# Kernel tuning notes

Hardware: AMD Instinct MI355X
Metric: run time of the kernel (lower is better)

Reference implementation:

```python
import jax, jax.numpy as jnp
import numpy as np

N1, E1, D_IN, D_OUT = 100000, 1600000, 128, 128
N2, E2, NB = 1024, 200000, 30


def setup_inputs() -> dict:
    key = jax.random.key(0)
    ks = jax.random.split(key, 11)
    return {
        "x_g1": jax.random.normal(ks[0], (N1, D_IN), jnp.float32),
        "W_stc": jax.random.normal(ks[1], (D_IN, D_OUT), jnp.float32) / np.sqrt(D_IN),
        "b_stc": jax.random.normal(ks[2], (D_OUT,), jnp.float32) * 0.01,
        "x_g2": jax.random.normal(ks[3], (N2, N2), jnp.float32),
        "basis": jax.random.normal(ks[4], (NB, N2, N2), jnp.float32) / np.sqrt(N2 * NB),
        "att": jax.random.normal(ks[5], (E2, NB), jnp.float32),
        "root": jax.random.normal(ks[6], (N2, N2), jnp.float32) / np.sqrt(N2),
        "bias_rgcn": jax.random.normal(ks[7], (N2,), jnp.float32) * 0.01,
        "edge_index_g1": jax.random.randint(ks[8], (2, E1), 0, N1, jnp.int64),
        "edge_index_g2": jax.random.randint(ks[9], (2, E2), 0, N2, jnp.int64),
        "edge_type_g2": jax.random.randint(ks[10], (E2,), 0, E2, jnp.int64),
    }


def reference(x_g1, W_stc, b_stc, x_g2, basis, att, root, bias_rgcn,
              edge_index_g1, edge_index_g2, edge_type_g2):
    # ---- STCConv on G1: mean-aggregate neighbor features, then linear ----
    src1, dst1 = edge_index_g1[0], edge_index_g1[1]
    deg1 = jax.ops.segment_sum(jnp.ones((E1,), x_g1.dtype), dst1, num_segments=N1)
    agg1 = jax.ops.segment_sum(x_g1[src1], dst1, num_segments=N1)  # [N1, D_IN]
    agg1 = agg1 / jnp.maximum(deg1, 1.0)[:, None]
    h1 = jax.nn.relu(agg1 @ W_stc + b_stc)
    out1 = jax.nn.log_softmax(h1, axis=1)

    # ---- RGCNConv on G2 with basis decomposition: W_r = sum_b att[r,b] B_b ----
    src2, dst2 = edge_index_g2[0], edge_index_g2[1]
    deg2 = jnp.maximum(
        jax.ops.segment_sum(jnp.ones((E2,), x_g2.dtype), dst2, num_segments=N2), 1.0)
    x_src = x_g2[src2]            # [E2, N2] gathered source features
    coeff = att[edge_type_g2]     # [E2, NB] per-edge basis coefficients
    h2 = x_g2 @ root + bias_rgcn  # root/self transform
    # aggregate per basis first (cheap [N2,N2] matmul after scatter)
    for b in range(NB):
        S = jax.ops.segment_sum(x_src * coeff[:, b:b + 1], dst2, num_segments=N2)
        h2 = h2 + (S / deg2[:, None]) @ basis[b]
    h2 = jax.nn.relu(h2)
    out2 = jax.nn.log_softmax(h2, axis=1)
    return (out1, out2)
```

## Files before the change

### kernel.cpp

```cpp
#include <hip/hip_runtime.h>

typedef unsigned short u16;
typedef unsigned int u32;
typedef unsigned long long u64;
typedef __attribute__((ext_vector_type(8))) short short8;
typedef __attribute__((ext_vector_type(4))) float floatx4;

#define NBMAX 2048

__device__ __forceinline__ float b2f(u16 u) {
    u32 x = ((u32)u) << 16; float f; __builtin_memcpy(&f, &x, 4); return f;
}
__device__ __forceinline__ u16 f2b(float f) {
    u32 x; __builtin_memcpy(&x, &f, 4);
    u32 r = (x + 0x7fffu + ((x >> 16) & 1u)) >> 16;
    return (u16)r;
}
__device__ __forceinline__ float ldf(const void* p, long i, int isf) {
    return isf ? ((const float*)p)[i] : b2f(((const u16*)p)[i]);
}
__device__ __forceinline__ void stf(void* p, long i, float v, int isf) {
    if (isf) ((float*)p)[i] = v; else ((u16*)p)[i] = f2b(v);
}
__device__ __forceinline__ int ldidx(const int* w, long i, int is64) {
    return is64 ? w[2 * i] : w[i];
}
__device__ __forceinline__ void gload16(const u16* g, u16* l) {
    __builtin_amdgcn_global_load_lds((const __attribute__((address_space(1))) void*)g,
                                     (__attribute__((address_space(3))) void*)l, 16, 0, 0);
}

__global__ void detect_kernel(const u32* __restrict__ xw, const u32* __restrict__ iw,
                              int* __restrict__ flags) {
    int lane = threadIdx.x;
    u32 w = xw[lane];
    u32 b1 = (w >> 8) & 0x7f;
    int isbf = (b1 >= 0x38 && b1 <= 0x41) ? 1 : 0;
    int cbf = __popcll(__ballot(isbf));
    u32 hi = iw[2 * lane + 1];
    int cz = __popcll(__ballot(hi == 0u));
    if (lane == 0) {
        flags[0] = (cbf < 32) ? 1 : 0;
        flags[1] = (cz >= 56) ? 1 : 0;
    }
}


__global__ void count_kernel(const int* __restrict__ eiw, int E, int* __restrict__ cnt,
                             const int* __restrict__ flags) {
    int e = blockIdx.x * 256 + threadIdx.x;
    if (e < E) atomicAdd(&cnt[ldidx(eiw, (long)E + e, flags[1])], 1);
}

__global__ __launch_bounds__(256)
void bcount_kernel(const int* __restrict__ eiw, int E, int chunk,
                   int* __restrict__ bcnt, int NB, const int* __restrict__ flags) {
    __shared__ int h[NBMAX];
    int t = threadIdx.x;
    for (int i = t; i < NB; i += 256) h[i] = 0;
    __syncthreads();
    int is64 = flags[1];
    int lo = blockIdx.x * chunk;
    int hi = lo + chunk; if (hi > E) hi = E;
    for (int e = lo + t; e < hi; e += 256)
        atomicAdd(&h[ldidx(eiw, (long)E + e, is64) >> 7], 1);
    __syncthreads();
    for (int i = t; i < NB; i += 256)
        if (h[i]) atomicAdd(&bcnt[i], h[i]);
}

__global__ void bscan_kernel(const int* __restrict__ bcnt, int* __restrict__ boff,
                             int* __restrict__ bcur, int NB) {
    __shared__ int sm[1024];
    int t = threadIdx.x;
    int a = (2 * t < NB) ? bcnt[2 * t] : 0;
    int b = (2 * t + 1 < NB) ? bcnt[2 * t + 1] : 0;
    int s = a + b;
    sm[t] = s;
    __syncthreads();
    for (int o = 1; o < 1024; o <<= 1) {
        int x = (t >= o) ? sm[t - o] : 0;
        __syncthreads();
        sm[t] += x;
        __syncthreads();
    }
    int ex = sm[t] - s;
    if (2 * t < NB) { boff[2 * t] = ex; bcur[2 * t] = ex; }
    if (2 * t + 1 < NB) { boff[2 * t + 1] = ex + a; bcur[2 * t + 1] = ex + a; }
    if (t == 1023) boff[NB] = sm[1023];
}

__global__ __launch_bounds__(256)
void bscatter_kernel(const int* __restrict__ eiw, int E, int chunk,
                     int* __restrict__ bcur, int NB, u32* __restrict__ pair,
                     const int* __restrict__ flags) {
    __shared__ int h[NBMAX];
    __shared__ int cur[NBMAX];
    int t = threadIdx.x;
    for (int i = t; i < NB; i += 256) h[i] = 0;
    __syncthreads();
    int is64 = flags[1];
    int lo = blockIdx.x * chunk;
    int hi = lo + chunk; if (hi > E) hi = E;
    for (int e = lo + t; e < hi; e += 256)
        atomicAdd(&h[ldidx(eiw, (long)E + e, is64) >> 7], 1);
    __syncthreads();
    for (int i = t; i < NB; i += 256) {
        int c = h[i];
        h[i] = c ? atomicAdd(&bcur[i], c) : 0;
        cur[i] = 0;
    }
    __syncthreads();
    for (int e = lo + t; e < hi; e += 256) {
        int src = ldidx(eiw, e, is64);
        int d = ldidx(eiw, (long)E + e, is64);
        int b = d >> 7;
        int p = atomicAdd(&cur[b], 1);
        pair[h[b] + p] = ((u32)(d & 127) << 25) | (u32)src;
    }
}

__global__ __launch_bounds__(256)
void bucketfill2_kernel(const u32* __restrict__ pair, const int* __restrict__ boff,
                        int NB, int N1, int* __restrict__ off1, int* __restrict__ elist) {
    __shared__ int cnt[128], pre[128], soff[128], cur[128];
    int b = blockIdx.x, t = threadIdx.x;
    int lo = boff[b], hi = boff[b + 1];
    if (t < 128) cnt[t] = 0;
    __syncthreads();
    for (int i = lo + t; i < hi; i += 256)
        atomicAdd(&cnt[pair[i] >> 25], 1);
    __syncthreads();
    if (t < 128) pre[t] = cnt[t];
    __syncthreads();
    for (int o = 1; o < 128; o <<= 1) {
        int x = (t >= o && t < 128) ? pre[t - o] : 0;
        __syncthreads();
        if (t < 128) pre[t] += x;
        __syncthreads();
    }
    int d0 = b << 7;
    if (t < 128) {
        int s = lo + pre[t] - cnt[t];
        soff[t] = s;
        cur[t] = 0;
        if (d0 + t < N1) off1[d0 + t] = s;
    }
    if (b == NB - 1 && t == 0) off1[N1] = hi;
    __syncthreads();
    for (int i = lo + t; i < hi; i += 256) {
        u32 v = pair[i];
        int dl = v >> 25;
        int p = atomicAdd(&cur[dl], 1);
        elist[soff[dl] + p] = (int)(v & 0x1FFFFFFu);
    }
}

__global__ void scan_block_kernel(const int* __restrict__ in, int* __restrict__ out,
                                  int* __restrict__ bsum, int n) {
    __shared__ int sm[1024];
    int t = threadIdx.x;
    int i = blockIdx.x * 1024 + t;
    int v = (i < n) ? in[i] : 0;
    sm[t] = v;
    __syncthreads();
    for (int o = 1; o < 1024; o <<= 1) {
        int x = (t >= o) ? sm[t - o] : 0;
        __syncthreads();
        sm[t] += x;
        __syncthreads();
    }
    if (i < n) out[i] = sm[t] - v;
    if (t == 1023) bsum[blockIdx.x] = sm[1023];
}

__global__ void scan_small_kernel(int* __restrict__ bsum, int nb) {
    __shared__ int sm[128];
    int t = threadIdx.x;
    int v = (t < nb) ? bsum[t] : 0;
    sm[t] = v;
    __syncthreads();
    for (int o = 1; o < 128; o <<= 1) {
        int x = (t >= o) ? sm[t - o] : 0;
        __syncthreads();
        sm[t] += x;
        __syncthreads();
    }
    if (t < nb) bsum[t] = sm[t] - v;
}

__global__ void scan_add_kernel(int* __restrict__ off, const int* __restrict__ bsum,
                                int n, int total) {
    int i = blockIdx.x * 1024 + threadIdx.x;
    if (i < n) off[i] += bsum[blockIdx.x];
    if (i == 0) off[n] = total;
}

__global__ void fill_kernel(const int* __restrict__ eiw, int E, const int* __restrict__ off,
                            int* __restrict__ cur, int* __restrict__ elist,
                            const int* __restrict__ flags) {
    int e = blockIdx.x * 256 + threadIdx.x;
    if (e < E) {
        int is64 = flags[1];
        int d = ldidx(eiw, (long)E + e, is64);
        int p = atomicAdd(&cur[d], 1);
        elist[off[d] + p] = ldidx(eiw, e, is64);
    }
}

__global__ void fill2_kernel(const int* __restrict__ ei, const int* __restrict__ et, int E,
                             const int* __restrict__ off, int* __restrict__ cur,
                             u32* __restrict__ elist, const int* __restrict__ flags) {
    int e = blockIdx.x * 256 + threadIdx.x;
    if (e < E) {
        int is64 = flags[1];
        int s = ldidx(ei, e, is64);
        int d = ldidx(ei, (long)E + e, is64);
        int t = ldidx(et, e, is64);
        int p = atomicAdd(&cur[d], 1);
        elist[off[d] + p] = (u32)s | ((u32)t << 10);
    }
}

__global__ void cvt4_kernel(const void* __restrict__ in, u64* __restrict__ out, long n4,
                            const int* __restrict__ flags) {
    long i = (long)blockIdx.x * 256 + threadIdx.x;
    if (i >= n4) return;
    if (flags[0]) {
        float4 v = ((const float4*)in)[i];
        out[i] = (u64)f2b(v.x) | ((u64)f2b(v.y) << 16) | ((u64)f2b(v.z) << 32) |
                 ((u64)f2b(v.w) << 48);
    } else {
        out[i] = ((const u64*)in)[i];
    }
}

__global__ void agg_kernel(const void* __restrict__ xraw, const u32* __restrict__ xb,
                           const int* __restrict__ off, const int* __restrict__ elist,
                           u32* __restrict__ aggbf, int N, const int* __restrict__ flags,
                           int useXB) {
    int node = blockIdx.x * 4 + (threadIdx.x >> 6);
    if (node >= N) return;
    int lane = threadIdx.x & 63;
    int b = off[node], e = off[node + 1];
    float a0 = 0.f, a1 = 0.f, c0 = 0.f, c1 = 0.f;
    if (useXB) {
        int i = b;
        for (; i + 4 <= e; i += 4) {
            int s0 = elist[i], s1 = elist[i + 1], s2 = elist[i + 2], s3 = elist[i + 3];
            u32 v0 = xb[(long)s0 * 64 + lane];
            u32 v1 = xb[(long)s1 * 64 + lane];
            u32 v2 = xb[(long)s2 * 64 + lane];
            u32 v3 = xb[(long)s3 * 64 + lane];
            a0 += b2f((u16)(v0 & 0xffffu)) + b2f((u16)(v2 & 0xffffu));
            a1 += b2f((u16)(v0 >> 16)) + b2f((u16)(v2 >> 16));
            c0 += b2f((u16)(v1 & 0xffffu)) + b2f((u16)(v3 & 0xffffu));
            c1 += b2f((u16)(v1 >> 16)) + b2f((u16)(v3 >> 16));
        }
        for (; i < e; i++) {
            u32 v = xb[(long)elist[i] * 64 + lane];
            a0 += b2f((u16)(v & 0xffffu));
            a1 += b2f((u16)(v >> 16));
        }
        a0 += c0; a1 += c1;
    } else if (flags[0]) {
        const float* xf = (const float*)xraw;
        for (int i = b; i < e; i++) {
            long s = elist[i];
            a0 += xf[s * 128 + 2 * lane];
            a1 += xf[s * 128 + 2 * lane + 1];
        }
    } else {
        const u32* xu = (const u32*)xraw;
        for (int i = b; i < e; i++) {
            u32 v = xu[(long)elist[i] * 64 + lane];
            a0 += b2f((u16)(v & 0xffffu));
            a1 += b2f((u16)(v >> 16));
        }
    }
    int dg = e - b; if (dg < 1) dg = 1;
    float inv = 1.0f / (float)dg;
    aggbf[(long)node * 64 + lane] = (u32)f2b(a0 * inv) | ((u32)f2b(a1 * inv) << 16);
}

__global__ void transpose_kernel(const void* __restrict__ in, long inOff,
                                 u16* __restrict__ out, int R, int C,
                                 const int* __restrict__ flags) {
    __shared__ u16 tile[32][33];
    int isf = flags[0];
    int tx = threadIdx.x, ty = threadIdx.y;
    int x = blockIdx.x * 32 + tx;
#pragma unroll
    for (int i = 0; i < 4; i++) {
        int y = blockIdx.y * 32 + ty + i * 8;
        long idx = inOff + (long)y * C + x;
        tile[ty + i * 8][tx] = isf ? f2b(((const float*)in)[idx]) : ((const u16*)in)[idx];
    }
    __syncthreads();
    int x2 = blockIdx.y * 32 + tx;
#pragma unroll
    for (int i = 0; i < 4; i++) {
        int y2 = blockIdx.x * 32 + ty + i * 8;
        out[(long)y2 * R + x2] = tile[tx][ty + i * 8];
    }
}

__global__ __launch_bounds__(256)
void scatterA_lds_kernel(const u32* __restrict__ elist, const int* __restrict__ off,
                         const void* __restrict__ att, u16* __restrict__ Abf,
                         int b0, int CH, const int* __restrict__ flags) {
    __shared__ float sA[15 * 1024];
    const int d = blockIdx.x, t = threadIdx.x;
    const int b = off[d], e = off[d + 1];
    int cnt = e - b; if (cnt < 1) cnt = 1;
    const float inv = 1.0f / (float)cnt;
    const int tot = CH << 10;
    for (int i = t; i < tot; i += 256) sA[i] = 0.f;
    __syncthreads();
    const int isf = flags[0];
    for (int i = b + t; i < e; i += 256) {
        u32 v = elist[i];
        int s = v & 1023;
        long tb = (long)(v >> 10) * 30 + b0;
        for (int bb = 0; bb < CH; bb++)
            atomicAdd(&sA[(bb << 10) + s], ldf(att, tb + bb, isf) * inv);
    }
    __syncthreads();
    const long obase = (long)d * 256 + t;
    for (int bb = 0; bb < CH; bb++) {
        int base = (bb << 10) + (t << 2);
        u64 p = (u64)f2b(sA[base]) | ((u64)f2b(sA[base + 1]) << 16) |
                ((u64)f2b(sA[base + 2]) << 32) | ((u64)f2b(sA[base + 3]) << 48);
        ((u64*)Abf)[(long)bb * 262144 + obase] = p;
    }
}

template <int MODE>
__global__ __launch_bounds__(256)
void gemm_bt(const u16* __restrict__ A, long aBatch,
             const u16* __restrict__ BT,
             float* __restrict__ Cf, void* __restrict__ Cb,
             const void* __restrict__ bias, const int* __restrict__ flags,
             int M, int lda, int ldb, int ldc,
             int colOffDim, long cBatch, int kSplitStride, int kLen) {
    __shared__ u16 As[4096];
    __shared__ u16 Bs[4096];
    __shared__ float sred[2][2][128];
    const int t = threadIdx.x;
    const int gx = gridDim.x, gy = gridDim.y;
    const int nwg = gx * gy * gridDim.z;
    const int bid = blockIdx.x + gx * (blockIdx.y + gy * blockIdx.z);
    const int q = nwg >> 3, r = nwg & 7;
    const int xcd = bid & 7, idx = bid >> 3;
    const int nbid = (xcd < r ? xcd * (q + 1) : r * (q + 1) + (xcd - r) * q) + idx;
    const int bx = nbid % gx;
    const int by = (nbid / gx) % gy;
    const int bz = nbid / (gx * gy);

    const int isf = flags[0];
    A += (long)bz * aBatch;
    const int kBase = bz * kSplitStride;
    const int row0 = bx * 128;
    const int n0 = by * 128;
    const int lane = t & 63, wave = t >> 6;
    const int wrow = (wave >> 1) * 64, wcol = (wave & 1) * 64;
    const int quad = lane >> 4, l16 = lane & 15;

    long aoff[2], boff[2];
    u16 *ldsA[2], *ldsB[2];
#pragma unroll
    for (int h = 0; h < 2; h++) {
        int r2 = h * 64 + wave * 16 + (lane >> 2);
        int clog = (lane & 3) ^ ((r2 >> 1) & 3);
        int ga = row0 + r2; if (ga >= M) ga = M - 1;
        aoff[h] = (long)ga * lda + clog * 8;
        boff[h] = (long)(n0 + r2) * ldb + clog * 8;
        ldsA[h] = &As[(h * 64 + wave * 16) * 32];
        ldsB[h] = &Bs[(h * 64 + wave * 16) * 32];
    }
    int aidx[4], bidx[4];
#pragma unroll
    for (int i = 0; i < 4; i++) {
        int ra = wrow + i * 16 + l16;
        aidx[i] = ra * 32 + ((quad ^ ((ra >> 1) & 3)) * 8);
        int rb = wcol + i * 16 + l16;
        bidx[i] = rb * 32 + ((quad ^ ((rb >> 1) & 3)) * 8);
    }

    floatx4 acc[4][4];
#pragma unroll
    for (int i = 0; i < 4; i++)
#pragma unroll
        for (int j = 0; j < 4; j++)
            acc[i][j] = (floatx4){0.f, 0.f, 0.f, 0.f};

    for (int kt = kBase; kt < kBase + kLen; kt += 32) {
        __syncthreads();
#pragma unroll
        for (int h = 0; h < 2; h++) {
            gload16(A + aoff[h] + kt, ldsA[h]);
            gload16(BT + boff[h] + kt, ldsB[h]);
        }
        __syncthreads();
        short8 af[4], bfr[4];
#pragma unroll
        for (int i = 0; i < 4; i++) {
            af[i]  = *(const short8*)&As[aidx[i]];
            bfr[i] = *(const short8*)&Bs[bidx[i]];
        }
#pragma unroll
        for (int i = 0; i < 4; i++)
#pragma unroll
            for (int j = 0; j < 4; j++)
                acc[i][j] = __builtin_amdgcn_mfma_f32_16x16x32_bf16(af[i], bfr[j], acc[i][j], 0, 0, 0);
    }

    if (MODE == 0) {
        const int colhalf = wave & 1;
        float bv[4];
#pragma unroll
        for (int j = 0; j < 4; j++)
            bv[j] = ldf(bias, wcol + j * 16 + l16, isf);
        float Mp[4][4];
#pragma unroll
        for (int i = 0; i < 4; i++)
#pragma unroll
            for (int rr = 0; rr < 4; rr++) {
                float m = 0.f;
#pragma unroll
                for (int j = 0; j < 4; j++) {
                    float v = fmaxf(acc[i][j][rr] + bv[j], 0.f);
                    acc[i][j][rr] = v;
                    m = fmaxf(m, v);
                }
#pragma unroll
                for (int o = 1; o < 16; o <<= 1) m = fmaxf(m, __shfl_xor(m, o, 64));
                if (l16 == 0) sred[0][colhalf][wrow + i * 16 + quad * 4 + rr] = m;
            }
        __syncthreads();
#pragma unroll
        for (int i = 0; i < 4; i++)
#pragma unroll
            for (int rr = 0; rr < 4; rr++) {
                int r2 = wrow + i * 16 + quad * 4 + rr;
                Mp[i][rr] = fmaxf(sred[0][0][r2], sred[0][1][r2]);
                float s = 0.f;
#pragma unroll
                for (int j = 0; j < 4; j++) s += __expf(acc[i][j][rr] - Mp[i][rr]);
#pragma unroll
                for (int o = 1; o < 16; o <<= 1) s += __shfl_xor(s, o, 64);
                if (l16 == 0) sred[1][colhalf][r2] = s;
            }
        __syncthreads();
#pragma unroll
        for (int i = 0; i < 4; i++)
#pragma unroll
            for (int rr = 0; rr < 4; rr++) {
                int r2 = wrow + i * 16 + quad * 4 + rr;
                long crow = (long)row0 + r2;
                if (crow < M) {
                    float lg = __logf(sred[1][0][r2] + sred[1][1][r2]);
#pragma unroll
                    for (int j = 0; j < 4; j++)
                        stf(Cb, crow * 128 + wcol + j * 16 + l16,
                            acc[i][j][rr] - Mp[i][rr] - lg, isf);
                }
            }
        return;
    }

    const long colOff = (long)bz * colOffDim;
    float* Cfp = Cf ? Cf + (long)bz * cBatch : nullptr;
#pragma unroll
    for (int i = 0; i < 4; i++)
#pragma unroll
        for (int j = 0; j < 4; j++)
#pragma unroll
            for (int r2 = 0; r2 < 4; r2++) {
                long crow = row0 + wrow + i * 16 + quad * 4 + r2;
                long ccol = n0 + wcol + j * 16 + l16;
                float v = acc[i][j][r2];
                if (MODE == 1) {
                    ((u16*)Cb)[crow * ldc + colOff + ccol] = f2b(v);
                } else if (MODE == 2) {
                    Cfp[crow * ldc + ccol] = v + ldf(bias, ccol, isf);
                } else if (MODE == 3) {
                    Cfp[crow * ldc + ccol] += v;
                } else {
                    Cfp[crow * ldc + ccol] = v;
                }
            }
}

__global__ void softmax2_kernel(const float* __restrict__ Zr, const float* __restrict__ Zp,
                                void* __restrict__ out, long outOff, int nsplit,
                                const int* __restrict__ flags) {
    int row = blockIdx.x;
    int t = threadIdx.x;
    __shared__ float red[4];
    float4 v = ((const float4*)Zr)[(long)row * 256 + t];
    for (int s = 0; s < nsplit; s++) {
        float4 p = ((const float4*)Zp)[(long)s * 262144 + (long)row * 256 + t];
        v.x += p.x; v.y += p.y; v.z += p.z; v.w += p.w;
    }
    float z[4] = {fmaxf(v.x, 0.f), fmaxf(v.y, 0.f), fmaxf(v.z, 0.f), fmaxf(v.w, 0.f)};
    float m = fmaxf(fmaxf(z[0], z[1]), fmaxf(z[2], z[3]));
#pragma unroll
    for (int o = 1; o < 64; o <<= 1) m = fmaxf(m, __shfl_xor(m, o, 64));
    int wave = t >> 6, lane = t & 63;
    if (lane == 0) red[wave] = m;
    __syncthreads();
    m = fmaxf(fmaxf(red[0], red[1]), fmaxf(red[2], red[3]));
    __syncthreads();
    float s4 = __expf(z[0] - m) + __expf(z[1] - m) + __expf(z[2] - m) + __expf(z[3] - m);
#pragma unroll
    for (int o = 1; o < 64; o <<= 1) s4 += __shfl_xor(s4, o, 64);
    if (lane == 0) red[wave] = s4;
    __syncthreads();
    float lg = __logf(red[0] + red[1] + red[2] + red[3]);
    long base = outOff + (long)row * 1024 + t * 4;
    if (flags[0]) {
        float4 o = {z[0] - m - lg, z[1] - m - lg, z[2] - m - lg, z[3] - m - lg};
        ((float4*)out)[base >> 2] = o;
    } else {
        u64 p = (u64)f2b(z[0] - m - lg) | ((u64)f2b(z[1] - m - lg) << 16) |
                ((u64)f2b(z[2] - m - lg) << 32) | ((u64)f2b(z[3] - m - lg) << 48);
        ((u64*)out)[base >> 2] = p;
    }
}


extern "C" void kernel_launch(void* const* d_in, const int* in_sizes, int n_in,
                              void* d_out, int out_size, void* d_ws, size_t ws_size,
                              hipStream_t stream) {
    const void* x_g1 = d_in[0];
    const void* W    = d_in[1];
    const void* bstc = d_in[2];
    const void* x_g2 = d_in[3];
    const void* basis= d_in[4];
    const void* att  = d_in[5];
    const void* root = d_in[6];
    const void* brg  = d_in[7];
    const int* ei1   = (const int*)d_in[8];
    const int* ei2   = (const int*)d_in[9];
    const int* et2   = (const int*)d_in[10];
    const int N1 = in_sizes[0] / 128;
    const int E1 = in_sizes[8] / 2;
    const int E2 = in_sizes[9] / 2;

    const size_t MB = 1ull << 20;
    const int cCH[7] = {15, 10, 6, 5, 3, 2, 1};
    const int cNS[7] = { 8,  8, 8, 8, 8, 4, 2};
    int CH = 1, NS = 1, USE_XB = 1;
    bool found = false;
    for (int pass = 0; pass < 2 && !found; pass++) {
        size_t floorP1 = pass == 0 ? 68 * MB : 42 * MB;
        for (int c = 0; c < 7; c++) {
            size_t chunk = (size_t)cCH[c] * 6 * MB;
            size_t scratch = chunk > floorP1 ? chunk : floorP1;
            size_t need = 11 * MB + (size_t)cNS[c] * 4 * MB + scratch;
            if (need <= ws_size) {
                CH = cCH[c]; NS = cNS[c]; USE_XB = (pass == 0); found = true; break;
            }
        }
    }
    if (!found) { CH = 1; NS = 1; USE_XB = 0; }
    const int NC = 30 / CH;
    const int kSp = CH * 1024 / NS;

    char* ws = (char*)d_ws;
    u16*   XT    = (u16*)(ws + 0);
    u16*   rootT = (u16*)(ws + 2 * MB);
    u16*   Xbf   = (u16*)(ws + 4 * MB);
    u16*   WT    = (u16*)(ws + 6 * MB);
    int*   deg2  = (int*)(ws + 6 * MB + 65536);
    int*   off2  = (int*)(ws + 6 * MB + 73728);
    int*   cur2  = (int*)(ws + 6 * MB + 81920);
    int*   bsum2 = (int*)(ws + 6 * MB + 90112);
    int*   flags = (int*)(ws + 6 * MB + 98304);
    u32*   elist2= (u32*)(ws + 6 * MB + 131072);
    float* Zr    = (float*)(ws + 7 * MB);
    float* Zp    = (float*)(ws + 11 * MB);
    char*  S     = ws + 11 * MB + (size_t)NS * 4 * MB;
    int* off1   = (int*)(S);
    int* bktCnt = (int*)(S + 512 * 1024);
    int* bktOff = (int*)(S + 544 * 1024);
    int* bktCur = (int*)(S + 576 * 1024);
    int* bsum   = (int*)(S + 608 * 1024);
    int* deg1f  = (int*)(S + 1 * MB);
    int* cur1f  = (int*)(S + 1536 * 1024);
    u32* pair1  = (u32*)(S + 2 * MB);
    int* elist  = (int*)(S + 9 * MB);
    u16* xg1b   = (u16*)(S + 16 * MB);
    u16* aggbf  = (u16*)(S + (USE_XB ? 42 * MB : 16 * MB));
    u16*   Abf   = (u16*)S;
    u16*   ST    = (u16*)(S + (size_t)CH * 2 * MB);
    u16*   basTc = (u16*)(S + (size_t)CH * 4 * MB);

    detect_kernel<<<1, 64, 0, stream>>>((const u32*)x_g1, (const u32*)ei1, flags);

    hipMemsetAsync(deg2, 0, 4096, stream);
    hipMemsetAsync(cur2, 0, 4096, stream);

    const int NB1 = (N1 + 127) >> 7;
    if (NB1 <= NBMAX) {
        hipMemsetAsync(bktCnt, 0, (size_t)(NB1 + 1) * 4, stream);
        const int chunk = 8192;
        const int nbk = (E1 + chunk - 1) / chunk;
        bcount_kernel<<<nbk, 256, 0, stream>>>(ei1, E1, chunk, bktCnt, NB1, flags);
        bscan_kernel<<<1, 1024, 0, stream>>>(bktCnt, bktOff, bktCur, NB1);
        bscatter_kernel<<<nbk, 256, 0, stream>>>(ei1, E1, chunk, bktCur, NB1, pair1, flags);
        bucketfill2_kernel<<<NB1, 256, 0, stream>>>(pair1, bktOff, NB1, N1, off1, elist);
    } else {
        hipMemsetAsync(deg1f, 0, 1048576, stream);
        count_kernel<<<(E1 + 255) / 256, 256, 0, stream>>>(ei1, E1, deg1f, flags);
        int nb1 = (N1 + 1023) / 1024;
        scan_block_kernel<<<nb1, 1024, 0, stream>>>(deg1f, off1, bsum, N1);
        scan_small_kernel<<<1, 128, 0, stream>>>(bsum, nb1);
        scan_add_kernel<<<nb1, 1024, 0, stream>>>(off1, bsum, N1, E1);
        fill_kernel<<<(E1 + 255) / 256, 256, 0, stream>>>(ei1, E1, off1, cur1f, elist, flags);
    }
    if (USE_XB) {
        long n4 = (long)N1 * 32;
        cvt4_kernel<<<(int)((n4 + 255) / 256), 256, 0, stream>>>(x_g1, (u64*)xg1b, n4, flags);
    }
    agg_kernel<<<(N1 + 3) / 4, 256, 0, stream>>>(x_g1, (const u32*)xg1b, off1, elist,
                                                 (u32*)aggbf, N1, flags, USE_XB);
    transpose_kernel<<<dim3(4, 4), dim3(32, 8), 0, stream>>>(W, 0, WT, 128, 128, flags);
    gemm_bt<0><<<dim3((N1 + 127) / 128, 1, 1), 256, 0, stream>>>(
        aggbf, 0, WT, nullptr, d_out, bstc, flags, N1, 128, 128, 128, 0, 0, 0, 128);

    count_kernel<<<(E2 + 255) / 256, 256, 0, stream>>>(ei2, E2, deg2, flags);
    scan_block_kernel<<<1, 1024, 0, stream>>>(deg2, off2, bsum2, 1024);
    scan_small_kernel<<<1, 128, 0, stream>>>(bsum2, 1);
    scan_add_kernel<<<1, 1024, 0, stream>>>(off2, bsum2, 1024, E2);
    fill2_kernel<<<(E2 + 255) / 256, 256, 0, stream>>>(ei2, et2, E2, off2, cur2,
                                                       elist2, flags);
    cvt4_kernel<<<1024, 256, 0, stream>>>(x_g2, (u64*)Xbf, 262144, flags);
    transpose_kernel<<<dim3(32, 32), dim3(32, 8), 0, stream>>>(x_g2, 0, XT, 1024, 1024, flags);
    transpose_kernel<<<dim3(32, 32), dim3(32, 8), 0, stream>>>(root, 0, rootT, 1024, 1024, flags);
    gemm_bt<2><<<dim3(8, 8, 1), 256, 0, stream>>>(
        Xbf, 0, rootT, Zr, nullptr, brg, flags, 1024, 1024, 1024, 1024, 0, 0, 0, 1024);

    for (int c = 0; c < NC; c++) {
        scatterA_lds_kernel<<<1024, 256, 0, stream>>>(elist2, off2, att, Abf,
                                                      c * CH, CH, flags);
        transpose_kernel<<<dim3(32, CH * 32), dim3(32, 8), 0, stream>>>(
            basis, (long)c * CH * 1048576, basTc, CH * 1024, 1024, flags);
        gemm_bt<1><<<dim3(8, 8, CH), 256, 0, stream>>>(
            Abf, 1048576, XT, nullptr, ST, nullptr, flags,
            1024, 1024, 1024, CH * 1024, 1024, 0, 0, 1024);
        if (c == 0) {
            gemm_bt<4><<<dim3(8, 8, NS), 256, 0, stream>>>(
                ST, 0, basTc, Zp, nullptr, nullptr, flags,
                1024, CH * 1024, CH * 1024, 1024, 0, 1048576, kSp, kSp);
        } else {
            gemm_bt<3><<<dim3(8, 8, NS), 256, 0, stream>>>(
                ST, 0, basTc, Zp, nullptr, nullptr, flags,
                1024, CH * 1024, CH * 1024, 1024, 0, 1048576, kSp, kSp);
        }
    }
    softmax2_kernel<<<1024, 256, 0, stream>>>(Zr, Zp, d_out, (long)N1 * 128, NS, flags);
}
```

Before: 882.7 us.

## Build G2 CSR with LDS-histogram bucket scatter and specialize the STC GEMM

Replaces the G2 CSR build (global-atomic count, three-kernel scan, per-edge global-atomic fill) with a block-local LDS histogram count, a single-kernel scan and a chunked scatter kernel. Each block reserves a range per destination with one global atomic and then places its edges using LDS atomics. This cuts global atomic contention on only 1024 destinations and removes several launches and memsets. It also moves the STC log-softmax GEMM into its own kernel that keeps all of B resident in LDS and reads A fragments directly from global memory, which drops the generic gemm's A staging and its sred allocation for the other modes.

```diff
diff --git a/kernel.cpp b/kernel.cpp
--- a/kernel.cpp
+++ b/kernel.cpp
@@ -46,15 +46,10 @@
 }
 
 
-__global__ void count_kernel(const int* __restrict__ eiw, int E, int* __restrict__ cnt,
-                             const int* __restrict__ flags) {
-    int e = blockIdx.x * 256 + threadIdx.x;
-    if (e < E) atomicAdd(&cnt[ldidx(eiw, (long)E + e, flags[1])], 1);
-}
-
 __global__ __launch_bounds__(256)
 void bcount_kernel(const int* __restrict__ eiw, int E, int chunk,
-                   int* __restrict__ bcnt, int NB, const int* __restrict__ flags) {
+                   int* __restrict__ bcnt, int NB, int shift,
+                   const int* __restrict__ flags) {
     __shared__ int h[NBMAX];
     int t = threadIdx.x;
     for (int i = t; i < NB; i += 256) h[i] = 0;
@@ -63,7 +58,7 @@
     int lo = blockIdx.x * chunk;
     int hi = lo + chunk; if (hi > E) hi = E;
     for (int e = lo + t; e < hi; e += 256)
-        atomicAdd(&h[ldidx(eiw, (long)E + e, is64) >> 7], 1);
+        atomicAdd(&h[ldidx(eiw, (long)E + e, is64) >> shift], 1);
     __syncthreads();
     for (int i = t; i < NB; i += 256)
         if (h[i]) atomicAdd(&bcnt[i], h[i]);
@@ -121,6 +116,36 @@
 }
 
 __global__ __launch_bounds__(256)
+void bscatter2_kernel(const int* __restrict__ ei, const int* __restrict__ et, int E,
+                      int chunk, int* __restrict__ bcur, u32* __restrict__ elist2,
+                      const int* __restrict__ flags) {
+    __shared__ int h[1024];
+    __shared__ int cur[1024];
+    int t = threadIdx.x;
+    for (int i = t; i < 1024; i += 256) h[i] = 0;
+    __syncthreads();
+    int is64 = flags[1];
+    int lo = blockIdx.x * chunk;
+    int hi = lo + chunk; if (hi > E) hi = E;
+    for (int e = lo + t; e < hi; e += 256)
+        atomicAdd(&h[ldidx(ei, (long)E + e, is64)], 1);
+    __syncthreads();
+    for (int i = t; i < 1024; i += 256) {
+        int c = h[i];
+        h[i] = c ? atomicAdd(&bcur[i], c) : 0;
+        cur[i] = 0;
+    }
+    __syncthreads();
+    for (int e = lo + t; e < hi; e += 256) {
+        int s = ldidx(ei, e, is64);
+        int d = ldidx(ei, (long)E + e, is64);
+        int ty = ldidx(et, e, is64);
+        int p = atomicAdd(&cur[d], 1);
+        elist2[h[d] + p] = (u32)s | ((u32)ty << 10);
+    }
+}
+
+__global__ __launch_bounds__(256)
 void bucketfill2_kernel(const u32* __restrict__ pair, const int* __restrict__ boff,
                         int NB, int N1, int* __restrict__ off1, int* __restrict__ elist) {
     __shared__ int cnt[128], pre[128], soff[128], cur[128];
@@ -154,6 +179,12 @@
         int p = atomicAdd(&cur[dl], 1);
         elist[soff[dl] + p] = (int)(v & 0x1FFFFFFu);
     }
+}
+
+__global__ void count_kernel(const int* __restrict__ eiw, int E, int* __restrict__ cnt,
+                             const int* __restrict__ flags) {
+    int e = blockIdx.x * 256 + threadIdx.x;
+    if (e < E) atomicAdd(&cnt[ldidx(eiw, (long)E + e, flags[1])], 1);
 }
 
 __global__ void scan_block_kernel(const int* __restrict__ in, int* __restrict__ out,
@@ -205,20 +236,6 @@
         int d = ldidx(eiw, (long)E + e, is64);
         int p = atomicAdd(&cur[d], 1);
         elist[off[d] + p] = ldidx(eiw, e, is64);
-    }
-}
-
-__global__ void fill2_kernel(const int* __restrict__ ei, const int* __restrict__ et, int E,
-                             const int* __restrict__ off, int* __restrict__ cur,
-                             u32* __restrict__ elist, const int* __restrict__ flags) {
-    int e = blockIdx.x * 256 + threadIdx.x;
-    if (e < E) {
-        int is64 = flags[1];
-        int s = ldidx(ei, e, is64);
-        int d = ldidx(ei, (long)E + e, is64);
-        int t = ldidx(et, e, is64);
-        int p = atomicAdd(&cur[d], 1);
-        elist[off[d] + p] = (u32)s | ((u32)t << 10);
     }
 }
 
@@ -335,6 +352,117 @@
     }
 }
 
+__global__ __launch_bounds__(256)
+void gemm_stc(const u16* __restrict__ A, const u16* __restrict__ BT,
+              void* __restrict__ Cb, const void* __restrict__ bias,
+              const int* __restrict__ flags, int M) {
+    __shared__ u16 Bs[4][4096];
+    __shared__ float sred[2][2][128];
+    const int t = threadIdx.x;
+    const int isf = flags[0];
+    const int row0 = blockIdx.x * 128;
+    const int lane = t & 63, wave = t >> 6;
+    const int wrow = (wave >> 1) * 64, wcol = (wave & 1) * 64;
+    const int quad = lane >> 4, l16 = lane & 15;
+
+#pragma unroll
+    for (int kt = 0; kt < 4; kt++) {
+#pragma unroll
+        for (int h = 0; h < 2; h++) {
+            int r2 = h * 64 + wave * 16 + (lane >> 2);
+            int clog = (lane & 3) ^ ((r2 >> 1) & 3);
+            gload16(BT + (long)r2 * 128 + kt * 32 + clog * 8,
+                    &Bs[kt][(h * 64 + wave * 16) * 32]);
+        }
+    }
+    u32 aoff[4];
+#pragma unroll
+    for (int i = 0; i < 4; i++) {
+        int ga = row0 + wrow + i * 16 + l16; if (ga >= M) ga = M - 1;
+        aoff[i] = (u32)ga * 128u + (u32)(quad * 8);
+    }
+    int bidx[4];
+#pragma unroll
+    for (int j = 0; j < 4; j++) {
+        int rb = wcol + j * 16 + l16;
+        bidx[j] = rb * 32 + ((quad ^ ((rb >> 1) & 3)) * 8);
+    }
+    floatx4 acc[4][4];
+#pragma unroll
+    for (int i = 0; i < 4; i++)
+#pragma unroll
+        for (int j = 0; j < 4; j++)
+            acc[i][j] = (floatx4){0.f, 0.f, 0.f, 0.f};
+    __syncthreads();
+
+#pragma unroll
+    for (int kt = 0; kt < 4; kt++) {
+        short8 af[4], bfr[4];
+#pragma unroll
+        for (int i = 0; i < 4; i++)
+            af[i] = *(const short8*)(A + aoff[i] + kt * 32);
+#pragma unroll
+        for (int j = 0; j < 4; j++)
+            bfr[j] = *(const short8*)&Bs[kt][bidx[j]];
+#pragma unroll
+        for (int i = 0; i < 4; i++)
+#pragma unroll
+            for (int j = 0; j < 4; j++)
+                acc[i][j] = __builtin_amdgcn_mfma_f32_16x16x32_bf16(af[i], bfr[j], acc[i][j], 0, 0, 0);
+    }
+
+    const int colhalf = wave & 1;
+    float bv[4];
+#pragma unroll
+    for (int j = 0; j < 4; j++)
+        bv[j] = ldf(bias, wcol + j * 16 + l16, isf);
+    float Mp[4][4];
+#pragma unroll
+    for (int i = 0; i < 4; i++)
+#pragma unroll
+        for (int rr = 0; rr < 4; rr++) {
+            float m = 0.f;
+#pragma unroll
+            for (int j = 0; j < 4; j++) {
+                float v = fmaxf(acc[i][j][rr] + bv[j], 0.f);
+                acc[i][j][rr] = v;
+                m = fmaxf(m, v);
+            }
+#pragma unroll
+            for (int o = 1; o < 16; o <<= 1) m = fmaxf(m, __shfl_xor(m, o, 64));
+            if (l16 == 0) sred[0][colhalf][wrow + i * 16 + quad * 4 + rr] = m;
+        }
+    __syncthreads();
+#pragma unroll
+    for (int i = 0; i < 4; i++)
+#pragma unroll
+        for (int rr = 0; rr < 4; rr++) {
+            int r2 = wrow + i * 16 + quad * 4 + rr;
+            Mp[i][rr] = fmaxf(sred[0][0][r2], sred[0][1][r2]);
+            float s = 0.f;
+#pragma unroll
+            for (int j = 0; j < 4; j++) s += __expf(acc[i][j][rr] - Mp[i][rr]);
+#pragma unroll
+            for (int o = 1; o < 16; o <<= 1) s += __shfl_xor(s, o, 64);
+            if (l16 == 0) sred[1][colhalf][r2] = s;
+        }
+    __syncthreads();
+#pragma unroll
+    for (int i = 0; i < 4; i++)
+#pragma unroll
+        for (int rr = 0; rr < 4; rr++) {
+            int r2 = wrow + i * 16 + quad * 4 + rr;
+            long crow = (long)row0 + r2;
+            if (crow < M) {
+                float lg = __logf(sred[1][0][r2] + sred[1][1][r2]);
+#pragma unroll
+                for (int j = 0; j < 4; j++)
+                    stf(Cb, crow * 128 + wcol + j * 16 + l16,
+                        acc[i][j][rr] - Mp[i][rr] - lg, isf);
+            }
+        }
+}
+
 template <int MODE>
 __global__ __launch_bounds__(256)
 void gemm_bt(const u16* __restrict__ A, long aBatch,
@@ -345,7 +473,6 @@
              int colOffDim, long cBatch, int kSplitStride, int kLen) {
     __shared__ u16 As[4096];
     __shared__ u16 Bs[4096];
-    __shared__ float sred[2][2][128];
     const int t = threadIdx.x;
     const int gx = gridDim.x, gy = gridDim.y;
     const int nwg = gx * gy * gridDim.z;
@@ -413,60 +540,6 @@
 #pragma unroll
             for (int j = 0; j < 4; j++)
                 acc[i][j] = __builtin_amdgcn_mfma_f32_16x16x32_bf16(af[i], bfr[j], acc[i][j], 0, 0, 0);
-    }
-
-    if (MODE == 0) {
-        const int colhalf = wave & 1;
-        float bv[4];
-#pragma unroll
-        for (int j = 0; j < 4; j++)
-            bv[j] = ldf(bias, wcol + j * 16 + l16, isf);
-        float Mp[4][4];
-#pragma unroll
-        for (int i = 0; i < 4; i++)
-#pragma unroll
-            for (int rr = 0; rr < 4; rr++) {
-                float m = 0.f;
-#pragma unroll
-                for (int j = 0; j < 4; j++) {
-                    float v = fmaxf(acc[i][j][rr] + bv[j], 0.f);
-                    acc[i][j][rr] = v;
-                    m = fmaxf(m, v);
-                }
-#pragma unroll
-                for (int o = 1; o < 16; o <<= 1) m = fmaxf(m, __shfl_xor(m, o, 64));
-                if (l16 == 0) sred[0][colhalf][wrow + i * 16 + quad * 4 + rr] = m;
-            }
-        __syncthreads();
-#pragma unroll
-        for (int i = 0; i < 4; i++)
-#pragma unroll
-            for (int rr = 0; rr < 4; rr++) {
-                int r2 = wrow + i * 16 + quad * 4 + rr;
-                Mp[i][rr] = fmaxf(sred[0][0][r2], sred[0][1][r2]);
-                float s = 0.f;
-#pragma unroll
-                for (int j = 0; j < 4; j++) s += __expf(acc[i][j][rr] - Mp[i][rr]);
-#pragma unroll
-                for (int o = 1; o < 16; o <<= 1) s += __shfl_xor(s, o, 64);
-                if (l16 == 0) sred[1][colhalf][r2] = s;
-            }
-        __syncthreads();
-#pragma unroll
-        for (int i = 0; i < 4; i++)
-#pragma unroll
-            for (int rr = 0; rr < 4; rr++) {
-                int r2 = wrow + i * 16 + quad * 4 + rr;
-                long crow = (long)row0 + r2;
-                if (crow < M) {
-                    float lg = __logf(sred[1][0][r2] + sred[1][1][r2]);
-#pragma unroll
-                    for (int j = 0; j < 4; j++)
-                        stf(Cb, crow * 128 + wcol + j * 16 + l16,
-                            acc[i][j][rr] - Mp[i][rr] - lg, isf);
-                }
-            }
-        return;
     }
 
     const long colOff = (long)bz * colOffDim;
@@ -576,7 +649,6 @@
     int*   deg2  = (int*)(ws + 6 * MB + 65536);
     int*   off2  = (int*)(ws + 6 * MB + 73728);
     int*   cur2  = (int*)(ws + 6 * MB + 81920);
-    int*   bsum2 = (int*)(ws + 6 * MB + 90112);
     int*   flags = (int*)(ws + 6 * MB + 98304);
     u32*   elist2= (u32*)(ws + 6 * MB + 131072);
     float* Zr    = (float*)(ws + 7 * MB);
@@ -600,14 +672,13 @@
     detect_kernel<<<1, 64, 0, stream>>>((const u32*)x_g1, (const u32*)ei1, flags);
 
     hipMemsetAsync(deg2, 0, 4096, stream);
-    hipMemsetAsync(cur2, 0, 4096, stream);
 
     const int NB1 = (N1 + 127) >> 7;
     if (NB1 <= NBMAX) {
         hipMemsetAsync(bktCnt, 0, (size_t)(NB1 + 1) * 4, stream);
         const int chunk = 8192;
         const int nbk = (E1 + chunk - 1) / chunk;
-        bcount_kernel<<<nbk, 256, 0, stream>>>(ei1, E1, chunk, bktCnt, NB1, flags);
+        bcount_kernel<<<nbk, 256, 0, stream>>>(ei1, E1, chunk, bktCnt, NB1, 7, flags);
         bscan_kernel<<<1, 1024, 0, stream>>>(bktCnt, bktOff, bktCur, NB1);
         bscatter_kernel<<<nbk, 256, 0, stream>>>(ei1, E1, chunk, bktCur, NB1, pair1, flags);
         bucketfill2_kernel<<<NB1, 256, 0, stream>>>(pair1, bktOff, NB1, N1, off1, elist);
@@ -627,15 +698,13 @@
     agg_kernel<<<(N1 + 3) / 4, 256, 0, stream>>>(x_g1, (const u32*)xg1b, off1, elist,
                                                  (u32*)aggbf, N1, flags, USE_XB);
     transpose_kernel<<<dim3(4, 4), dim3(32, 8), 0, stream>>>(W, 0, WT, 128, 128, flags);
-    gemm_bt<0><<<dim3((N1 + 127) / 128, 1, 1), 256, 0, stream>>>(
-        aggbf, 0, WT, nullptr, d_out, bstc, flags, N1, 128, 128, 128, 0, 0, 0, 128);
-
-    count_kernel<<<(E2 + 255) / 256, 256, 0, stream>>>(ei2, E2, deg2, flags);
-    scan_block_kernel<<<1, 1024, 0, stream>>>(deg2, off2, bsum2, 1024);
-    scan_small_kernel<<<1, 128, 0, stream>>>(bsum2, 1);
-    scan_add_kernel<<<1, 1024, 0, stream>>>(off2, bsum2, 1024, E2);
-    fill2_kernel<<<(E2 + 255) / 256, 256, 0, stream>>>(ei2, et2, E2, off2, cur2,
-                                                       elist2, flags);
+    gemm_stc<<<dim3((N1 + 127) / 128), 256, 0, stream>>>(aggbf, WT, d_out, bstc, flags, N1);
+
+    const int chunk2 = 8192;
+    const int nbk2 = (E2 + chunk2 - 1) / chunk2;
+    bcount_kernel<<<nbk2, 256, 0, stream>>>(ei2, E2, chunk2, deg2, 1024, 0, flags);
+    bscan_kernel<<<1, 1024, 0, stream>>>(deg2, off2, cur2, 1024);
+    bscatter2_kernel<<<nbk2, 256, 0, stream>>>(ei2, et2, E2, chunk2, cur2, elist2, flags);
     cvt4_kernel<<<1024, 256, 0, stream>>>(x_g2, (u64*)Xbf, 262144, flags);
     transpose_kernel<<<dim3(32, 32), dim3(32, 8), 0, stream>>>(x_g2, 0, XT, 1024, 1024, flags);
     transpose_kernel<<<dim3(32, 32), dim3(32, 8), 0, stream>>>(root, 0, rootT, 1024, 1024, flags);
```

Result: faster. 832.3 us (-5.7%).
